# Performance work log

Hardware: AMD Instinct MI355X
Metric: run time of the kernel (lower is better)

Reference implementation:

```python
import jax, jax.numpy as jnp
import numpy as np

D_MODEL = 2048
D_INNER = 4096
D_STATE = 16
DT_RANK = 128
D_CONV = 4
EPS = 1e-5


def setup_inputs() -> dict:
    key = jax.random.key(0)
    ks = jax.random.split(key, 10)
    b, l = 1, 1024
    s = 0.02
    x = jax.random.normal(ks[0], (b, l, D_MODEL), jnp.float32)
    w_norm = jnp.ones((D_MODEL,), jnp.float32)
    W_in = jax.random.normal(ks[1], (D_MODEL, 2 * D_INNER), jnp.float32) * s
    conv_w = jax.random.normal(ks[2], (D_CONV, D_INNER), jnp.float32) * 0.3
    conv_b = jnp.zeros((D_INNER,), jnp.float32)
    W_xp = jax.random.normal(ks[3], (D_INNER, DT_RANK + 2 * D_STATE), jnp.float32) * s
    W_dt = jax.random.normal(ks[4], (DT_RANK, D_INNER), jnp.float32) * s
    b_dt = jnp.full((D_INNER,), -4.0, jnp.float32)  # softplus(-4) ~ small dt
    A_log = jnp.log(jnp.tile(jnp.arange(1, D_STATE + 1, dtype=jnp.float32), (D_INNER, 1)))
    D = jnp.ones((D_INNER,), jnp.float32)
    W_out = jax.random.normal(ks[5], (D_INNER, D_MODEL), jnp.float32) * s
    return dict(x=x, w_norm=w_norm, W_in=W_in, conv_w=conv_w, conv_b=conv_b,
                W_xp=W_xp, W_dt=W_dt, b_dt=b_dt, A_log=A_log, D=D, W_out=W_out)


def _rmsnorm(x, w):
    return x * jax.lax.rsqrt(jnp.mean(jnp.square(x), axis=-1, keepdims=True) + EPS) * w


def _depthwise_causal_conv(x, conv_w, conv_b):
    # x: (b, l, d_inner), conv_w: (d_conv, d_inner)
    k = conv_w[:, None, :]  # (W, I/groups=1, O)
    y = jax.lax.conv_general_dilated(
        x, k, window_strides=(1,), padding=((D_CONV - 1, 0),),
        dimension_numbers=('NWC', 'WIO', 'NWC'), feature_group_count=D_INNER)
    return y + conv_b


def _selective_scan(u, delta, A, B, C, D):
    # u, delta: (b,l,d); A: (d,n); B,C: (b,l,n); D: (d,)
    deltaA = jnp.exp(jnp.einsum('bld,dn->bldn', delta, A))          # (b,l,d,n)
    deltaBu = jnp.einsum('bld,bln,bld->bldn', delta, B, u)          # (b,l,d,n)
    dA = jnp.moveaxis(deltaA, 1, 0)    # (l,b,d,n)
    dBu = jnp.moveaxis(deltaBu, 1, 0)  # (l,b,d,n)
    Ct = jnp.moveaxis(C, 1, 0)         # (l,b,n)
    b, l, d = u.shape
    n = A.shape[1]

    def step(h, inputs):
        dA_t, dBu_t, C_t = inputs
        h = h * dA_t + dBu_t                       # (b,d,n)
        y = jnp.einsum('bdn,bn->bd', h, C_t)       # (b,d)
        return h, y

    h0 = jnp.zeros((b, d, n), u.dtype)
    _, ys = jax.lax.scan(step, h0, (dA, dBu, Ct))
    y = jnp.moveaxis(ys, 0, 1)                     # (b,l,d)
    return y + u * D


def reference(x, w_norm, W_in, conv_w, conv_b, W_xp, W_dt, b_dt, A_log, D, W_out):
    # ResidualBlock: out = MambaBlock(RMSNorm(x)) + x
    xn = _rmsnorm(x, w_norm)
    xz = xn @ W_in                                  # (b,l,2*d_inner)
    xs, res = jnp.split(xz, 2, axis=-1)
    xs = _depthwise_causal_conv(xs, conv_w, conv_b)
    xs = jax.nn.silu(xs)
    # SSM
    A = -jnp.exp(A_log)                             # (d_inner, n)
    xdbc = xs @ W_xp                                # (b,l,dt_rank+2n)
    dt_r = xdbc[..., :DT_RANK]
    B = xdbc[..., DT_RANK:DT_RANK + D_STATE]
    C = xdbc[..., DT_RANK + D_STATE:]
    delta = jax.nn.softplus(dt_r @ W_dt + b_dt)     # (b,l,d_inner)
    y = _selective_scan(xs, delta, A, B, C, D)
    y = y * jax.nn.silu(res)
    out = y @ W_out + x
    return out
```

## Files before the change

### kernel.cpp

```cpp
#include <hip/hip_runtime.h>
#include <math.h>

#define L_SEQ   1024
#define DMODEL  2048
#define DINNER  4096
#define DSTATE  16
#define DTRANK  128
#define N_XZ    (2 * DINNER)
#define N_XP    (DTRANK + 2 * DSTATE)
#define EPS_F   1e-5f
#define NCHUNK  32
#define TCH     32
#define SK_XP   16
#define SK_OUT  2

using bf16x8 = __attribute__((ext_vector_type(8))) short;
using f32x4  = __attribute__((ext_vector_type(4))) float;

__device__ __forceinline__ float silu_f(float v) {
    return v * (1.0f / (1.0f + __expf(-v)));
}
__device__ __forceinline__ float softplus_f(float v) {
    return (v > 15.0f) ? v : log1pf(__expf(v));
}
__device__ __forceinline__ unsigned short f2bf(float f) {
    unsigned b = __float_as_uint(f);
    return (unsigned short)((b + 0x7FFFu + ((b >> 16) & 1u)) >> 16);
}
__device__ __forceinline__ float bf2f(unsigned short u) {
    return __uint_as_float((unsigned)u << 16);
}

#define GLOAD_LDS(gp, lp) \
    __builtin_amdgcn_global_load_lds((const __attribute__((address_space(1))) void*)(gp), \
                                     (__attribute__((address_space(3))) void*)(lp), 16, 0, 0)

__device__ __forceinline__ void transpose_body(const float* __restrict__ W,
                                               unsigned short* __restrict__ BT,
                                               int K, int N, int bx, int by,
                                               unsigned short (*Tl)[72]) {
    const int k0 = by * 64, n0 = bx * 32;
    const int kr = threadIdx.x >> 3;
    const int nc = (threadIdx.x & 7) * 4;
    float4 v0 = *(const float4*)&W[(size_t)(k0 + kr) * N + n0 + nc];
    float4 v1 = *(const float4*)&W[(size_t)(k0 + kr + 32) * N + n0 + nc];
    Tl[nc + 0][kr] = f2bf(v0.x); Tl[nc + 1][kr] = f2bf(v0.y);
    Tl[nc + 2][kr] = f2bf(v0.z); Tl[nc + 3][kr] = f2bf(v0.w);
    Tl[nc + 0][kr + 32] = f2bf(v1.x); Tl[nc + 1][kr + 32] = f2bf(v1.y);
    Tl[nc + 2][kr + 32] = f2bf(v1.z); Tl[nc + 3][kr + 32] = f2bf(v1.w);
    __syncthreads();
    const int n = threadIdx.x >> 3;
    const int k8 = (threadIdx.x & 7) * 8;
    *(bf16x8*)&BT[(size_t)(n0 + n) * K + k0 + k8] = *(const bf16x8*)&Tl[n][k8];
}

__global__ __launch_bounds__(256) void prep_kernel(const float* __restrict__ W_in,
                                                   const float* __restrict__ W_xp,
                                                   const float* __restrict__ W_dt,
                                                   const float* __restrict__ W_out,
                                                   const float* __restrict__ x,
                                                   const float* __restrict__ wn,
                                                   unsigned short* __restrict__ BT_in,
                                                   unsigned short* __restrict__ BTxp,
                                                   unsigned short* __restrict__ BTdt,
                                                   unsigned short* __restrict__ BT_out,
                                                   unsigned short* __restrict__ xn_bf) {
    __shared__ unsigned short Tl[32][72];
    __shared__ float red[4];
    int b = blockIdx.x;
    if (b < 8192) {
        transpose_body(W_in, BT_in, DMODEL, N_XZ, b % 256, b / 256, Tl);
    } else if (b < 12288) {
        b -= 8192;
        transpose_body(W_out, BT_out, DINNER, DMODEL, b % 64, b / 64, Tl);
    } else if (b < 12608) {
        b -= 12288;
        transpose_body(W_xp, BTxp, DINNER, N_XP, b % 5, b / 5, Tl);
    } else if (b < 12864) {
        b -= 12608;
        transpose_body(W_dt, BTdt, DTRANK, DINNER, b % 128, b / 128, Tl);
    } else {
        const int row = b - 12864;
        const float4* xr = (const float4*)(x + (size_t)row * DMODEL);
        float ss = 0.f;
        float4 v0 = xr[threadIdx.x];
        float4 v1 = xr[threadIdx.x + 256];
        ss += v0.x*v0.x + v0.y*v0.y + v0.z*v0.z + v0.w*v0.w;
        ss += v1.x*v1.x + v1.y*v1.y + v1.z*v1.z + v1.w*v1.w;
        #pragma unroll
        for (int o = 32; o > 0; o >>= 1) ss += __shfl_down(ss, o);
        const int lane = threadIdx.x & 63, wv = threadIdx.x >> 6;
        if (lane == 0) red[wv] = ss;
        __syncthreads();
        if (threadIdx.x == 0) {
            float t = red[0] + red[1] + red[2] + red[3];
            red[0] = rsqrtf(t / (float)DMODEL + EPS_F);
        }
        __syncthreads();
        const float scale = red[0];
        const float4* wr = (const float4*)wn;
        float4 w0 = wr[threadIdx.x];
        float4 w1 = wr[threadIdx.x + 256];
        ushort4 o0, o1;
        o0.x = f2bf(v0.x * scale * w0.x); o0.y = f2bf(v0.y * scale * w0.y);
        o0.z = f2bf(v0.z * scale * w0.z); o0.w = f2bf(v0.w * scale * w0.w);
        o1.x = f2bf(v1.x * scale * w1.x); o1.y = f2bf(v1.y * scale * w1.y);
        o1.z = f2bf(v1.z * scale * w1.z); o1.w = f2bf(v1.w * scale * w1.w);
        unsigned short* outr = xn_bf + (size_t)row * DMODEL;
        *(ushort4*)&outr[threadIdx.x * 4] = o0;
        *(ushort4*)&outr[1024 + threadIdx.x * 4] = o1;
    }
}

template <int BM, int BN, int OUTM>
__global__ __launch_bounds__(256) void gemm_mfma_kernel(const unsigned short* __restrict__ A,
                                                        const unsigned short* __restrict__ BT,
                                                        void* __restrict__ Cv,
                                                        int K, int Kc, int ldc, int Ncols,
                                                        const float* __restrict__ bias) {
    constexpr int MT = BM / 32;
    constexpr int NT = BN / 32;
    __shared__ __align__(16) unsigned short Al[BM * 32];
    __shared__ __align__(16) unsigned short Bl[BN * 32];
    const int tid = threadIdx.x;
    const int lane = tid & 63, wave = tid >> 6;
    const int wm = wave >> 1, wn = wave & 1;
    const int bm = blockIdx.y * BM, bn = blockIdx.x * BN;
    const size_t koff = (size_t)blockIdx.z * Kc;
    const size_t zCoff = (size_t)blockIdx.z * (size_t)gridDim.y * BM * ldc;
    const int sr = lane >> 2;
    const int sk = (((lane & 3) ^ ((sr >> 1) & 3))) * 8;
    const int fr = lane & 15;
    const int fq = lane >> 4;
    const int fsw = (fq ^ ((fr >> 1) & 3)) * 8;

    f32x4 acc[MT][NT];
    #pragma unroll
    for (int i = 0; i < MT; ++i)
        #pragma unroll
        for (int j = 0; j < NT; ++j)
            acc[i][j] = (f32x4){0.f, 0.f, 0.f, 0.f};

    for (int k0 = 0; k0 < Kc; k0 += 32) {
        #pragma unroll
        for (int is = wave; is < BM / 16; is += 4)
            GLOAD_LDS(&A[(size_t)(bm + is * 16 + sr) * K + koff + k0 + sk], &Al[is * 512]);
        #pragma unroll
        for (int is = wave; is < BN / 16; is += 4)
            GLOAD_LDS(&BT[(size_t)(bn + is * 16 + sr) * K + koff + k0 + sk], &Bl[is * 512]);
        __syncthreads();
        bf16x8 af[MT], bfr[NT];
        #pragma unroll
        for (int i = 0; i < MT; ++i)
            af[i] = *(const bf16x8*)&Al[(wm * (BM / 2) + i * 16 + fr) * 32 + fsw];
        #pragma unroll
        for (int j = 0; j < NT; ++j)
            bfr[j] = *(const bf16x8*)&Bl[(wn * (BN / 2) + j * 16 + fr) * 32 + fsw];
        #pragma unroll
        for (int i = 0; i < MT; ++i)
            #pragma unroll
            for (int j = 0; j < NT; ++j)
                acc[i][j] = __builtin_amdgcn_mfma_f32_16x16x32_bf16(af[i], bfr[j], acc[i][j], 0, 0, 0);
        __syncthreads();
    }

    #pragma unroll
    for (int i = 0; i < MT; ++i) {
        const int row = bm + wm * (BM / 2) + i * 16 + fq * 4;
        #pragma unroll
        for (int j = 0; j < NT; ++j) {
            const int col = bn + wn * (BN / 2) + j * 16 + fr;
            if (col < Ncols) {
                #pragma unroll
                for (int r = 0; r < 4; ++r) {
                    float v = acc[i][j][r];
                    if (OUTM == 0) {
                        ((unsigned short*)Cv)[(size_t)(row + r) * ldc + col] = f2bf(v);
                    } else if (OUTM == 1) {
                        ((unsigned short*)Cv)[(size_t)(row + r) * ldc + col] =
                            f2bf(softplus_f(v + bias[col]));
                    } else {
                        ((float*)Cv + zCoff)[(size_t)(row + r) * ldc + col] = v;
                    }
                }
            }
        }
    }
}

__global__ __launch_bounds__(256) void conv_silu_kernel(const unsigned short* __restrict__ xz_bf,
                                                        const float* __restrict__ cw,
                                                        const float* __restrict__ cb,
                                                        unsigned short* __restrict__ xs_bf) {
    const int idx = blockIdx.x * 256 + threadIdx.x;
    const int t = idx >> 12;
    const int c = idx & (DINNER - 1);
    float acc = cb[c];
    #pragma unroll
    for (int k = 0; k < 4; ++k) {
        const int tt = t + k - 3;
        if (tt >= 0) acc = fmaf(bf2f(xz_bf[(size_t)tt * N_XZ + c]), cw[k * DINNER + c], acc);
    }
    xs_bf[idx] = f2bf(silu_f(acc));
}

__global__ __launch_bounds__(256) void reduce_sk_kernel(const float* __restrict__ part,
                                                        float* __restrict__ xdbc,
                                                        unsigned short* __restrict__ xdbc_dt) {
    const int i = blockIdx.x * 256 + threadIdx.x;
    float s = 0.f;
    #pragma unroll
    for (int c = 0; c < SK_XP; ++c) s += part[(size_t)c * (L_SEQ * N_XP) + i];
    xdbc[i] = s;
    const int col = i % N_XP;
    if (col < DTRANK) xdbc_dt[(i / N_XP) * DTRANK + col] = f2bf(s);
}

__global__ __launch_bounds__(256) void reduce_out_kernel(const float* __restrict__ part,
                                                         const float* __restrict__ x,
                                                         float* __restrict__ out) {
    const int i = blockIdx.x * 256 + threadIdx.x;
    float4 a = ((const float4*)part)[i];
    float4 b = ((const float4*)(part + (size_t)L_SEQ * DMODEL))[i];
    float4 r = ((const float4*)x)[i];
    float4 o;
    o.x = a.x + b.x + r.x; o.y = a.y + b.y + r.y;
    o.z = a.z + b.z + r.z; o.w = a.w + b.w + r.w;
    ((float4*)out)[i] = o;
}

__global__ __launch_bounds__(256) void scan_pass1(const unsigned short* __restrict__ delta_bf,
                                                  const unsigned short* __restrict__ xs_bf,
                                                  const float* __restrict__ xdbc,
                                                  const float* __restrict__ A_log,
                                                  float* __restrict__ S,
                                                  float* __restrict__ sumdl) {
    __shared__ float BC[TCH][32];
    const int c = blockIdx.y;
    const int d = blockIdx.x * 256 + threadIdx.x;
    const int t0 = c * TCH;
    {
        const int tt = threadIdx.x >> 3, q = threadIdx.x & 7;
        *(float4*)&BC[tt][q * 4] =
            *(const float4*)&xdbc[(size_t)(t0 + tt) * N_XP + DTRANK + q * 4];
    }
    __syncthreads();
    float Aa[16];
    #pragma unroll
    for (int n = 0; n < 16; ++n) Aa[n] = -__expf(A_log[d * 16 + n]);
    float h[16];
    #pragma unroll
    for (int n = 0; n < 16; ++n) h[n] = 0.f;
    float sd = 0.f;
    for (int t = 0; t < TCH; ++t) {
        const float dl = bf2f(delta_bf[(size_t)(t0 + t) * DINNER + d]);
        const float u  = bf2f(xs_bf[(size_t)(t0 + t) * DINNER + d]);
        sd += dl;
        const float du = dl * u;
        #pragma unroll
        for (int n = 0; n < 16; ++n)
            h[n] = fmaf(h[n], __expf(dl * Aa[n]), du * BC[t][n]);
    }
    float* Sp = &S[((size_t)c * DINNER + d) * 16];
    #pragma unroll
    for (int n = 0; n < 16; n += 4)
        *(float4*)&Sp[n] = make_float4(h[n], h[n + 1], h[n + 2], h[n + 3]);
    sumdl[c * DINNER + d] = sd;
}

__global__ __launch_bounds__(256) void scan_pass2(const float* __restrict__ S,
                                                  const float* __restrict__ sumdl,
                                                  const float* __restrict__ A_log,
                                                  float* __restrict__ h0) {
    const int i = blockIdx.x * 256 + threadIdx.x;
    const int dd = i >> 4;
    const float A = -__expf(A_log[i]);
    float h = 0.f;
    #pragma unroll
    for (int c = 0; c < NCHUNK; ++c) {
        h0[(size_t)c * (DINNER * 16) + i] = h;
        h = h * __expf(A * sumdl[c * DINNER + dd]) + S[(size_t)c * (DINNER * 16) + i];
    }
}

__global__ __launch_bounds__(256) void scan_pass3(const unsigned short* __restrict__ delta_bf,
                                                  const unsigned short* __restrict__ xs_bf,
                                                  const float* __restrict__ xdbc,
                                                  const unsigned short* __restrict__ xz_bf,
                                                  const float* __restrict__ A_log,
                                                  const float* __restrict__ Dp,
                                                  const float* __restrict__ h0,
                                                  unsigned short* __restrict__ yg_bf) {
    __shared__ float BC[TCH][32];
    const int c = blockIdx.y;
    const int d = blockIdx.x * 256 + threadIdx.x;
    const int t0 = c * TCH;
    {
        const int tt = threadIdx.x >> 3, q = threadIdx.x & 7;
        *(float4*)&BC[tt][q * 4] =
            *(const float4*)&xdbc[(size_t)(t0 + tt) * N_XP + DTRANK + q * 4];
    }
    __syncthreads();
    float Aa[16];
    #pragma unroll
    for (int n = 0; n < 16; ++n) Aa[n] = -__expf(A_log[d * 16 + n]);
    float h[16];
    const float* h0p = &h0[(size_t)c * (DINNER * 16) + d * 16];
    #pragma unroll
    for (int n = 0; n < 16; n += 4) {
        float4 v = *(const float4*)&h0p[n];
        h[n] = v.x; h[n + 1] = v.y; h[n + 2] = v.z; h[n + 3] = v.w;
    }
    const float Dd = Dp[d];
    for (int t = 0; t < TCH; ++t) {
        const float dl = bf2f(delta_bf[(size_t)(t0 + t) * DINNER + d]);
        const float u  = bf2f(xs_bf[(size_t)(t0 + t) * DINNER + d]);
        const float du = dl * u;
        float y = 0.f;
        #pragma unroll
        for (int n = 0; n < 16; ++n) {
            h[n] = fmaf(h[n], __expf(dl * Aa[n]), du * BC[t][n]);
            y = fmaf(h[n], BC[t][16 + n], y);
        }
        const float res = bf2f(xz_bf[(size_t)(t0 + t) * N_XZ + DINNER + d]);
        yg_bf[(size_t)(t0 + t) * DINNER + d] = f2bf((y + u * Dd) * silu_f(res));
    }
}

extern "C" void kernel_launch(void* const* d_in, const int* in_sizes, int n_in,
                              void* d_out, int out_size, void* d_ws, size_t ws_size,
                              hipStream_t stream) {
    const float* x     = (const float*)d_in[0];
    const float* wn    = (const float*)d_in[1];
    const float* W_in  = (const float*)d_in[2];
    const float* cw    = (const float*)d_in[3];
    const float* cb    = (const float*)d_in[4];
    const float* W_xp  = (const float*)d_in[5];
    const float* W_dt  = (const float*)d_in[6];
    const float* b_dt  = (const float*)d_in[7];
    const float* A_log = (const float*)d_in[8];
    const float* Dp    = (const float*)d_in[9];
    const float* W_out = (const float*)d_in[10];
    float* out = (float*)d_out;

    float* ws = (float*)d_ws;
    unsigned short* xz_bf    = (unsigned short*)ws;
    unsigned short* xs_bf    = (unsigned short*)(ws + 4194304);
    unsigned short* yg_bf    = (unsigned short*)(ws + 6291456);
    unsigned short* delta_bf = (unsigned short*)(ws + 8388608);
    float*          part     = ws + 10485760;
    float*          S        = part;
    float*          sumdl    = S + 2097152;
    float*          h0       = ws + 13107200;
    float*          xdbc     = ws + 15204352;
    unsigned short* xn_bf    = (unsigned short*)(ws + 15368192);
    unsigned short* BTxp     = (unsigned short*)(ws + 16416768);
    unsigned short* BTdt     = (unsigned short*)(ws + 16744448);
    unsigned short* xdbc_dt  = (unsigned short*)(ws + 17006592);
    unsigned short* BT_in    = (unsigned short*)(ws + 17072128);
    unsigned short* BT_out   = (unsigned short*)(ws + 25460736);
    float*          part_out = ws + 8388608;

    prep_kernel<<<13888, 256, 0, stream>>>(W_in, W_xp, W_dt, W_out, x, wn,
                                           BT_in, BTxp, BTdt, BT_out, xn_bf);
    gemm_mfma_kernel<128, 128, 0><<<dim3(N_XZ / 128, L_SEQ / 128), 256, 0, stream>>>(
        xn_bf, BT_in, xz_bf, DMODEL, DMODEL, N_XZ, N_XZ, nullptr);
    conv_silu_kernel<<<(L_SEQ * DINNER) / 256, 256, 0, stream>>>(xz_bf, cw, cb, xs_bf);
    gemm_mfma_kernel<128, 64, 2><<<dim3(3, L_SEQ / 128, SK_XP), 256, 0, stream>>>(
        xs_bf, BTxp, part, DINNER, DINNER / SK_XP, N_XP, N_XP, nullptr);
    reduce_sk_kernel<<<(L_SEQ * N_XP) / 256, 256, 0, stream>>>(part, xdbc, xdbc_dt);
    gemm_mfma_kernel<64, 64, 1><<<dim3(DINNER / 64, L_SEQ / 64), 256, 0, stream>>>(
        xdbc_dt, BTdt, delta_bf, DTRANK, DTRANK, DINNER, DINNER, b_dt);
    scan_pass1<<<dim3(DINNER / 256, NCHUNK), 256, 0, stream>>>(delta_bf, xs_bf, xdbc, A_log, S, sumdl);
    scan_pass2<<<(DINNER * 16) / 256, 256, 0, stream>>>(S, sumdl, A_log, h0);
    scan_pass3<<<dim3(DINNER / 256, NCHUNK), 256, 0, stream>>>(delta_bf, xs_bf, xdbc, xz_bf,
                                                               A_log, Dp, h0, yg_bf);
    gemm_mfma_kernel<64, 64, 2><<<dim3(DMODEL / 64, L_SEQ / 64, SK_OUT), 256, 0, stream>>>(
        yg_bf, BT_out, part_out, DINNER, DINNER / SK_OUT, DMODEL, DMODEL, nullptr);
    reduce_out_kernel<<<(L_SEQ * DMODEL / 4) / 256, 256, 0, stream>>>(part_out, x, out);
}
```

Measured before the change: 340.0 us.

## Deepen GEMM K-step per barrier, retile GEMMs, fuse residual add into out-projection

The MFMA GEMM now stages KC=2 slices of 32 along K into LDS per barrier pair, halving synchronisation per unit of K work at the cost of doubled LDS. The input projection and xproj GEMMs switch to 64-row tiles, giving more blocks. The output projection drops its split-K partials and separate reduce kernel and adds the residual x directly in the GEMM epilogue. This saves a launch and the partial-buffer round trip but loses the split-K parallelism on the final GEMM.

```diff
diff --git a/kernel.cpp b/kernel.cpp
--- a/kernel.cpp
+++ b/kernel.cpp
@@ -12,7 +12,6 @@
 #define NCHUNK  32
 #define TCH     32
 #define SK_XP   16
-#define SK_OUT  2
 
 using bf16x8 = __attribute__((ext_vector_type(8))) short;
 using f32x4  = __attribute__((ext_vector_type(4))) float;
@@ -112,22 +111,23 @@
     }
 }
 
-template <int BM, int BN, int OUTM>
+template <int BM, int BN, int KC, int OUTM>
 __global__ __launch_bounds__(256) void gemm_mfma_kernel(const unsigned short* __restrict__ A,
                                                         const unsigned short* __restrict__ BT,
                                                         void* __restrict__ Cv,
                                                         int K, int Kc, int ldc, int Ncols,
-                                                        const float* __restrict__ bias) {
+                                                        const float* __restrict__ aux) {
     constexpr int MT = BM / 32;
     constexpr int NT = BN / 32;
-    __shared__ __align__(16) unsigned short Al[BM * 32];
-    __shared__ __align__(16) unsigned short Bl[BN * 32];
+    __shared__ __align__(16) unsigned short Al[KC * BM * 32];
+    __shared__ __align__(16) unsigned short Bl[KC * BN * 32];
     const int tid = threadIdx.x;
     const int lane = tid & 63, wave = tid >> 6;
     const int wm = wave >> 1, wn = wave & 1;
     const int bm = blockIdx.y * BM, bn = blockIdx.x * BN;
     const size_t koff = (size_t)blockIdx.z * Kc;
-    const size_t zCoff = (size_t)blockIdx.z * (size_t)gridDim.y * BM * ldc;
+    float* Cf = (float*)Cv;
+    if (OUTM == 2) Cf += (size_t)blockIdx.z * (size_t)gridDim.y * BM * ldc;
     const int sr = lane >> 2;
     const int sk = (((lane & 3) ^ ((sr >> 1) & 3))) * 8;
     const int fr = lane & 15;
@@ -141,26 +141,34 @@
         for (int j = 0; j < NT; ++j)
             acc[i][j] = (f32x4){0.f, 0.f, 0.f, 0.f};
 
-    for (int k0 = 0; k0 < Kc; k0 += 32) {
-        #pragma unroll
-        for (int is = wave; is < BM / 16; is += 4)
-            GLOAD_LDS(&A[(size_t)(bm + is * 16 + sr) * K + koff + k0 + sk], &Al[is * 512]);
-        #pragma unroll
-        for (int is = wave; is < BN / 16; is += 4)
-            GLOAD_LDS(&BT[(size_t)(bn + is * 16 + sr) * K + koff + k0 + sk], &Bl[is * 512]);
+    for (int k0 = 0; k0 < Kc; k0 += 32 * KC) {
+        #pragma unroll
+        for (int p = 0; p < KC; ++p) {
+            #pragma unroll
+            for (int is = wave; is < BM / 16; is += 4)
+                GLOAD_LDS(&A[(size_t)(bm + is * 16 + sr) * K + koff + k0 + p * 32 + sk],
+                          &Al[p * BM * 32 + is * 512]);
+            #pragma unroll
+            for (int is = wave; is < BN / 16; is += 4)
+                GLOAD_LDS(&BT[(size_t)(bn + is * 16 + sr) * K + koff + k0 + p * 32 + sk],
+                          &Bl[p * BN * 32 + is * 512]);
+        }
         __syncthreads();
-        bf16x8 af[MT], bfr[NT];
-        #pragma unroll
-        for (int i = 0; i < MT; ++i)
-            af[i] = *(const bf16x8*)&Al[(wm * (BM / 2) + i * 16 + fr) * 32 + fsw];
-        #pragma unroll
-        for (int j = 0; j < NT; ++j)
-            bfr[j] = *(const bf16x8*)&Bl[(wn * (BN / 2) + j * 16 + fr) * 32 + fsw];
-        #pragma unroll
-        for (int i = 0; i < MT; ++i)
+        #pragma unroll
+        for (int p = 0; p < KC; ++p) {
+            bf16x8 af[MT], bfr[NT];
+            #pragma unroll
+            for (int i = 0; i < MT; ++i)
+                af[i] = *(const bf16x8*)&Al[p * BM * 32 + (wm * (BM / 2) + i * 16 + fr) * 32 + fsw];
             #pragma unroll
             for (int j = 0; j < NT; ++j)
-                acc[i][j] = __builtin_amdgcn_mfma_f32_16x16x32_bf16(af[i], bfr[j], acc[i][j], 0, 0, 0);
+                bfr[j] = *(const bf16x8*)&Bl[p * BN * 32 + (wn * (BN / 2) + j * 16 + fr) * 32 + fsw];
+            #pragma unroll
+            for (int i = 0; i < MT; ++i)
+                #pragma unroll
+                for (int j = 0; j < NT; ++j)
+                    acc[i][j] = __builtin_amdgcn_mfma_f32_16x16x32_bf16(af[i], bfr[j], acc[i][j], 0, 0, 0);
+        }
         __syncthreads();
     }
 
@@ -178,9 +186,12 @@
                         ((unsigned short*)Cv)[(size_t)(row + r) * ldc + col] = f2bf(v);
                     } else if (OUTM == 1) {
                         ((unsigned short*)Cv)[(size_t)(row + r) * ldc + col] =
-                            f2bf(softplus_f(v + bias[col]));
+                            f2bf(softplus_f(v + aux[col]));
+                    } else if (OUTM == 2) {
+                        Cf[(size_t)(row + r) * ldc + col] = v;
                     } else {
-                        ((float*)Cv + zCoff)[(size_t)(row + r) * ldc + col] = v;
+                        Cf[(size_t)(row + r) * ldc + col] =
+                            v + aux[(size_t)(row + r) * ldc + col];
                     }
                 }
             }
@@ -214,19 +225,6 @@
     xdbc[i] = s;
     const int col = i % N_XP;
     if (col < DTRANK) xdbc_dt[(i / N_XP) * DTRANK + col] = f2bf(s);
-}
-
-__global__ __launch_bounds__(256) void reduce_out_kernel(const float* __restrict__ part,
-                                                         const float* __restrict__ x,
-                                                         float* __restrict__ out) {
-    const int i = blockIdx.x * 256 + threadIdx.x;
-    float4 a = ((const float4*)part)[i];
-    float4 b = ((const float4*)(part + (size_t)L_SEQ * DMODEL))[i];
-    float4 r = ((const float4*)x)[i];
-    float4 o;
-    o.x = a.x + b.x + r.x; o.y = a.y + b.y + r.y;
-    o.z = a.z + b.z + r.z; o.w = a.w + b.w + r.w;
-    ((float4*)out)[i] = o;
 }
 
 __global__ __launch_bounds__(256) void scan_pass1(const unsigned short* __restrict__ delta_bf,
@@ -349,33 +347,31 @@
     unsigned short* yg_bf    = (unsigned short*)(ws + 6291456);
     unsigned short* delta_bf = (unsigned short*)(ws + 8388608);
     float*          part     = ws + 10485760;
-    float*          S        = part;
-    float*          sumdl    = S + 2097152;
-    float*          h0       = ws + 13107200;
-    float*          xdbc     = ws + 15204352;
-    unsigned short* xn_bf    = (unsigned short*)(ws + 15368192);
-    unsigned short* BTxp     = (unsigned short*)(ws + 16416768);
-    unsigned short* BTdt     = (unsigned short*)(ws + 16744448);
-    unsigned short* xdbc_dt  = (unsigned short*)(ws + 17006592);
-    unsigned short* BT_in    = (unsigned short*)(ws + 17072128);
-    unsigned short* BT_out   = (unsigned short*)(ws + 25460736);
-    float*          part_out = ws + 8388608;
+    float*          S        = ws + 13107200;
+    float*          sumdl    = ws + 15204352;
+    float*          h0       = ws + 15335424;
+    float*          xdbc     = ws + 17432576;
+    unsigned short* xn_bf    = (unsigned short*)(ws + 17596416);
+    unsigned short* BTxp     = (unsigned short*)(ws + 18644992);
+    unsigned short* BTdt     = (unsigned short*)(ws + 18972672);
+    unsigned short* xdbc_dt  = (unsigned short*)(ws + 19234816);
+    unsigned short* BT_in    = (unsigned short*)(ws + 19300352);
+    unsigned short* BT_out   = (unsigned short*)(ws + 27688960);
 
     prep_kernel<<<13888, 256, 0, stream>>>(W_in, W_xp, W_dt, W_out, x, wn,
                                            BT_in, BTxp, BTdt, BT_out, xn_bf);
-    gemm_mfma_kernel<128, 128, 0><<<dim3(N_XZ / 128, L_SEQ / 128), 256, 0, stream>>>(
+    gemm_mfma_kernel<64, 128, 2, 0><<<dim3(N_XZ / 128, L_SEQ / 64), 256, 0, stream>>>(
         xn_bf, BT_in, xz_bf, DMODEL, DMODEL, N_XZ, N_XZ, nullptr);
     conv_silu_kernel<<<(L_SEQ * DINNER) / 256, 256, 0, stream>>>(xz_bf, cw, cb, xs_bf);
-    gemm_mfma_kernel<128, 64, 2><<<dim3(3, L_SEQ / 128, SK_XP), 256, 0, stream>>>(
+    gemm_mfma_kernel<64, 64, 2, 2><<<dim3(3, L_SEQ / 64, SK_XP), 256, 0, stream>>>(
         xs_bf, BTxp, part, DINNER, DINNER / SK_XP, N_XP, N_XP, nullptr);
     reduce_sk_kernel<<<(L_SEQ * N_XP) / 256, 256, 0, stream>>>(part, xdbc, xdbc_dt);
-    gemm_mfma_kernel<64, 64, 1><<<dim3(DINNER / 64, L_SEQ / 64), 256, 0, stream>>>(
+    gemm_mfma_kernel<64, 64, 2, 1><<<dim3(DINNER / 64, L_SEQ / 64), 256, 0, stream>>>(
         xdbc_dt, BTdt, delta_bf, DTRANK, DTRANK, DINNER, DINNER, b_dt);
     scan_pass1<<<dim3(DINNER / 256, NCHUNK), 256, 0, stream>>>(delta_bf, xs_bf, xdbc, A_log, S, sumdl);
     scan_pass2<<<(DINNER * 16) / 256, 256, 0, stream>>>(S, sumdl, A_log, h0);
     scan_pass3<<<dim3(DINNER / 256, NCHUNK), 256, 0, stream>>>(delta_bf, xs_bf, xdbc, xz_bf,
                                                                A_log, Dp, h0, yg_bf);
-    gemm_mfma_kernel<64, 64, 2><<<dim3(DMODEL / 64, L_SEQ / 64, SK_OUT), 256, 0, stream>>>(
-        yg_bf, BT_out, part_out, DINNER, DINNER / SK_OUT, DMODEL, DMODEL, nullptr);
-    reduce_out_kernel<<<(L_SEQ * DMODEL / 4) / 256, 256, 0, stream>>>(part_out, x, out);
-}
+    gemm_mfma_kernel<64, 64, 2, 3><<<dim3(DMODEL / 64, L_SEQ / 64), 256, 0, stream>>>(
+        yg_bf, BT_out, out, DINNER, DINNER, DMODEL, DMODEL, x);
+}
```

Result: no change. 336.9 us (-0.9%).
